# Performance work log

Hardware: AMD Instinct MI355X
Metric: run time of the kernel (lower is better)

## Reference

```python
import jax, jax.numpy as jnp
import numpy as np

D_MODEL = 1024
NUM_HEADS = 16
D_K = D_MODEL // NUM_HEADS


def setup_inputs() -> dict:
    key = jax.random.key(0)
    ks = jax.random.split(key, 9)
    B, S = 4, 2048
    scale = 1.0 / np.sqrt(D_MODEL)
    x = jax.random.normal(ks[0], (B, S, D_MODEL), dtype=jnp.float32)
    wq = jax.random.normal(ks[1], (D_MODEL, D_MODEL), dtype=jnp.float32) * scale
    wk = jax.random.normal(ks[2], (D_MODEL, D_MODEL), dtype=jnp.float32) * scale
    wv = jax.random.normal(ks[3], (D_MODEL, D_MODEL), dtype=jnp.float32) * scale
    wo = jax.random.normal(ks[4], (D_MODEL, D_MODEL), dtype=jnp.float32) * scale
    bq = jax.random.normal(ks[5], (D_MODEL,), dtype=jnp.float32) * 0.01
    bk = jax.random.normal(ks[6], (D_MODEL,), dtype=jnp.float32) * 0.01
    bv = jax.random.normal(ks[7], (D_MODEL,), dtype=jnp.float32) * 0.01
    bo = jax.random.normal(ks[8], (D_MODEL,), dtype=jnp.float32) * 0.01
    return {"x": x, "wq": wq, "bq": bq, "wk": wk, "bk": bk,
            "wv": wv, "bv": bv, "wo": wo, "bo": bo}


def reference(x, wq, bq, wk, bk, wv, bv, wo, bo):
    B, S, _ = x.shape
    # projections -> [B, H, S, d_k]
    def split_heads(t):
        return t.reshape(B, S, NUM_HEADS, D_K).transpose(0, 2, 1, 3)
    q = split_heads(x @ wq.T + bq)
    k = split_heads(x @ wk.T + bk)
    v = split_heads(x @ wv.T + bv)
    scores = jnp.einsum("bhqd,bhkd->bhqk", q, k) / np.sqrt(D_K).astype(np.float32)
    attn = jax.nn.softmax(scores, axis=-1)  # dropout is identity at eval
    out = jnp.einsum("bhqk,bhkd->bhqd", attn, v)
    out = out.transpose(0, 2, 1, 3).reshape(B, S, D_MODEL)
    return out @ wo.T + bo
```

## Files before the change

kernel.cpp:

```cpp
#include <hip/hip_runtime.h>

#define D_MODEL 1024
#define NHEADS  16
#define DK      64
#define BATCH   4
#define SEQ     2048
#define MROWS   (BATCH*SEQ)
#define BHCOUNT (BATCH*NHEADS)
#define KTILES  (SEQ/64)

typedef _Float16 half8 __attribute__((ext_vector_type(8)));
typedef _Float16 half4 __attribute__((ext_vector_type(4)));
typedef float    floatx4 __attribute__((ext_vector_type(4)));
typedef float    floatx16 __attribute__((ext_vector_type(16)));

__device__ __forceinline__ void load_lds16(const void* g, void* l) {
    __builtin_amdgcn_global_load_lds((const __attribute__((address_space(1))) void*)g,
                                     (__attribute__((address_space(3))) void*)l, 16, 0, 0);
}

__device__ __forceinline__ unsigned pkrtz_u32(float a, float b) {
    auto h = __builtin_amdgcn_cvt_pkrtz(a, b);
    union { decltype(h) v; unsigned u; } c; c.v = h; return c.u;
}

__device__ __forceinline__ int permrow(int r) {
    return (r & ~12) | ((r & 4) << 1) | ((r & 8) >> 1);
}

__global__ __launch_bounds__(256)
void cvt_f32_f16(const float* __restrict__ in, _Float16* __restrict__ out) {
    size_t i = ((size_t)blockIdx.x*256 + threadIdx.x)*4;
    float4 v = *(const float4*)(in + i);
    half4 h = {(_Float16)v.x, (_Float16)v.y, (_Float16)v.z, (_Float16)v.w};
    *(half4*)(out + i) = h;
}

__global__ __launch_bounds__(256)
void cvt4_f32_f16(const float* __restrict__ a, const float* __restrict__ b,
                  const float* __restrict__ c, const float* __restrict__ d,
                  _Float16* __restrict__ oa, _Float16* __restrict__ ob,
                  _Float16* __restrict__ oc, _Float16* __restrict__ od) {
    const float* src; _Float16* dst;
    switch (blockIdx.y) {
        case 0:  src=a; dst=oa; break;
        case 1:  src=b; dst=ob; break;
        case 2:  src=c; dst=oc; break;
        default: src=d; dst=od; break;
    }
    size_t i = ((size_t)blockIdx.x*256 + threadIdx.x)*4;
    float4 v = *(const float4*)(src + i);
    half4 h = {(_Float16)v.x, (_Float16)v.y, (_Float16)v.z, (_Float16)v.w};
    *(half4*)(dst + i) = h;
}

template<int MODE, int BK>
__global__ __launch_bounds__(256)
void gemm_nt_f16(const _Float16* __restrict__ A, const _Float16* __restrict__ W,
                 const float* __restrict__ b0, const float* __restrict__ b1,
                 const float* __restrict__ b2, void* __restrict__ Cout, float qscale)
{
    constexpr int GR  = BK/8;
    constexpr int NIT = BK/16;
    constexpr int NKT = 1024/BK;
    constexpr int KS  = BK/32;
    __shared__ _Float16 As[2][128*BK];
    __shared__ _Float16 Ws[2][128*BK];
    const int t = threadIdx.x;
    const int w = t >> 6, l = t & 63;
    const int wm = w >> 1, wn = w & 1;

    const int L   = blockIdx.x + (int)gridDim.x * blockIdx.y;
    const int nbx = gridDim.x;
    const int x   = L & 7;
    const int k   = L >> 3;
    const int cpc = (nbx + 7) >> 3;
    const int bn  = (x*cpc + (k % cpc)) * 128;
    const int bm  = (k / cpc) * 128;

    const int lrow = l & 15, lq4 = l >> 4;

    int srow[NIT], scol[NIT];
    #pragma unroll
    for (int it = 0; it < NIT; ++it) {
        int s = (it*4 + w)*64 + l;
        int r = s / GR, g = s % GR, gs;
        if constexpr (BK == 64) gs = g ^ (r & 7);
        else                    gs = g ^ ((r >> 1) & 3);
        srow[it] = r; scol[it] = gs*8;
    }

    floatx4 acc[4][4];
    #pragma unroll
    for (int i = 0; i < 4; ++i)
        #pragma unroll
        for (int j = 0; j < 4; ++j) acc[i][j] = (floatx4){0.f,0.f,0.f,0.f};

    #pragma unroll
    for (int it = 0; it < NIT; ++it) {
        load_lds16(A + (size_t)(bm + srow[it])*1024 + scol[it], &As[0][(it*4+w)*512]);
        load_lds16(W + (size_t)(bn + srow[it])*1024 + scol[it], &Ws[0][(it*4+w)*512]);
    }

    for (int kt = 0; kt < NKT; ++kt) {
        __syncthreads();
        const int cur = kt & 1;
        if (kt + 1 < NKT) {
            const int k1 = (kt + 1)*BK;
            #pragma unroll
            for (int it = 0; it < NIT; ++it) {
                load_lds16(A + (size_t)(bm + srow[it])*1024 + k1 + scol[it], &As[cur^1][(it*4+w)*512]);
                load_lds16(W + (size_t)(bn + srow[it])*1024 + k1 + scol[it], &Ws[cur^1][(it*4+w)*512]);
            }
        }
        #pragma unroll
        for (int ks = 0; ks < KS; ++ks) {
            int xg;
            if constexpr (BK == 64) xg = ((ks*4 + lq4) ^ (lrow & 7))*8;
            else                    xg = (lq4 ^ ((lrow >> 1) & 3))*8;
            half8 af[4], bf[4];
            #pragma unroll
            for (int i = 0; i < 4; ++i) af[i] = *(half8*)&As[cur][(wm*64 + i*16 + lrow)*BK + xg];
            #pragma unroll
            for (int j = 0; j < 4; ++j) bf[j] = *(half8*)&Ws[cur][(wn*64 + j*16 + lrow)*BK + xg];
            __builtin_amdgcn_s_setprio(1);
            #pragma unroll
            for (int i = 0; i < 4; ++i)
                #pragma unroll
                for (int j = 0; j < 4; ++j)
                    acc[i][j] = __builtin_amdgcn_mfma_f32_16x16x32_f16(af[i], bf[j], acc[i][j], 0, 0, 0);
            __builtin_amdgcn_s_setprio(0);
        }
    }

    constexpr size_t NXc = (size_t)MROWS * D_MODEL;
    const int which = bn >> 10;
    const float* bptr = (which == 0) ? b0 : (which == 1) ? b1 : b2;
    const float scale = (which == 0) ? qscale : 1.0f;
    #pragma unroll
    for (int j = 0; j < 4; ++j) {
        int gcol = bn + wn*64 + j*16 + lrow;
        float bv = bptr[gcol & 1023];
        #pragma unroll
        for (int i = 0; i < 4; ++i) {
            #pragma unroll
            for (int r = 0; r < 4; ++r) {
                int gm = bm + wm*64 + i*16 + lq4*4 + r;
                float val = (acc[i][j][r] + bv) * scale;
                if (MODE == 0) {
                    ((float*)Cout)[(size_t)gm*1024 + gcol] = val;
                } else {
                    int hc = gcol & 1023;
                    int b = gm >> 11, s = gm & 2047;
                    int h = hc >> 6, dk = hc & 63;
                    ((_Float16*)Cout)[which*NXc + (((size_t)(b*NHEADS + h))*SEQ + s)*DK + dk] = (_Float16)val;
                }
            }
        }
    }
}

__global__ __launch_bounds__(256)
void transpose_v(const _Float16* __restrict__ V, _Float16* __restrict__ Vt)
{
    __shared__ unsigned Lt[64][33];
    const int t = threadIdx.x;
    const int bh = blockIdx.y;
    const int s0 = blockIdx.x*64;
    const _Float16* Vb = V + ((size_t)bh*SEQ + s0)*DK;
    const int sp = t >> 3, dkc = (t & 7)*8;
    uint4 r0 = *(const uint4*)(Vb + (2*sp+0)*64 + dkc);
    uint4 r1 = *(const uint4*)(Vb + (2*sp+1)*64 + dkc);
    unsigned a0[4] = {r0.x, r0.y, r0.z, r0.w};
    unsigned a1[4] = {r1.x, r1.y, r1.z, r1.w};
    #pragma unroll
    for (int i = 0; i < 4; ++i) {
        Lt[dkc+2*i+0][sp] = (a0[i] & 0xFFFFu) | (a1[i] << 16);
        Lt[dkc+2*i+1][sp] = (a0[i] >> 16)     | (a1[i] & 0xFFFF0000u);
    }
    __syncthreads();
    const int dk = t >> 2, spc = (t & 3)*8;
    uint4 o0 = {Lt[dk][spc+0], Lt[dk][spc+1], Lt[dk][spc+2], Lt[dk][spc+3]};
    uint4 o1 = {Lt[dk][spc+4], Lt[dk][spc+5], Lt[dk][spc+6], Lt[dk][spc+7]};
    _Float16* dst = Vt + ((size_t)bh*DK + dk)*SEQ + s0 + spc*2;
    *(uint4*)(dst)     = o0;
    *(uint4*)(dst + 8) = o1;
}

__global__ __launch_bounds__(128)
void attn_mfma(const _Float16* __restrict__ Q, const _Float16* __restrict__ K,
               const _Float16* __restrict__ Vt, _Float16* __restrict__ AO)
{
    __shared__ _Float16 Ks[2][64*64];
    __shared__ _Float16 Vs[2][64*64];

    const int t = threadIdx.x;
    const int w = t >> 6, l = t & 63;
    const int l31 = l & 31, hi = l >> 5;

    const int L   = blockIdx.x + (int)gridDim.x * blockIdx.y;
    const int wid = (L & 7) * 128 + (L >> 3);
    const int bh  = wid >> 4;
    const int q0  = (wid & 15) * 128;

    const _Float16* Qb = Q  + ((size_t)bh*SEQ + q0)*DK;
    const _Float16* Kb = K  + (size_t)bh*SEQ*DK;
    const _Float16* Vb = Vt + (size_t)bh*DK*SEQ;

    int srow[4], scol[4], karow[4];
    #pragma unroll
    for (int it = 0; it < 4; ++it) {
        int s = (it*2 + w)*64 + l;
        int r = s >> 3;
        int lc = (s & 7) ^ (r & 7);
        srow[it] = r; scol[it] = lc*8;
        karow[it] = permrow(r);
    }

    half8 qf[2][4];
    #pragma unroll
    for (int qt = 0; qt < 2; ++qt)
        #pragma unroll
        for (int kk = 0; kk < 4; ++kk)
            qf[qt][kk] = *(const half8*)(Qb + (size_t)(w*64 + qt*32 + l31)*DK + kk*16 + hi*8);

    #pragma unroll
    for (int it = 0; it < 4; ++it) {
        load_lds16(Kb + (size_t)karow[it]*DK + scol[it], &Ks[0][(it*2+w)*512]);
        load_lds16(Vb + (size_t)srow[it]*SEQ + scol[it], &Vs[0][(it*2+w)*512]);
    }

    floatx16 Oacc[2][2];
    #pragma unroll
    for (int qt = 0; qt < 2; ++qt)
        #pragma unroll
        for (int i = 0; i < 16; ++i) { Oacc[qt][0][i] = 0.f; Oacc[qt][1][i] = 0.f; }
    float psum[2] = {0.f, 0.f};
    floatx16 z16;
    #pragma unroll
    for (int i = 0; i < 16; ++i) z16[i] = 0.f;

#define ATTN_PREFETCH(NBUF, KT1)                                                          \
    if ((KT1) < KTILES) {                                                                 \
        _Pragma("unroll")                                                                 \
        for (int it = 0; it < 4; ++it) {                                                  \
            load_lds16(Kb + ((size_t)((KT1)*64 + karow[it]))*DK + scol[it],               \
                       &Ks[NBUF][(it*2+w)*512]);                                          \
            load_lds16(Vb + (size_t)srow[it]*SEQ + (KT1)*64 + scol[it],                   \
                       &Vs[NBUF][(it*2+w)*512]);                                          \
        }                                                                                 \
    }

#define ATTN_STEP(CUR, KT)                                                                \
    {                                                                                     \
        __syncthreads();                                                                  \
        ATTN_PREFETCH((CUR)^1, (KT)+1)                                                    \
        _Pragma("unroll")                                                                 \
        for (int kb = 0; kb < 2; ++kb) {                                                  \
            const int row = kb*32 + l31;                                                  \
                                \
            floatx16 sTa, sTb;                                                            \
            {                                                                             \
                half8 kf = *(half8*)&Ks[CUR][row*64 + ((hi ^ (row & 7)))*8];              \
                sTa = __builtin_amdgcn_mfma_f32_32x32x16_f16(kf, qf[0][0], z16, 0, 0, 0); \
                sTb = __builtin_amdgcn_mfma_f32_32x32x16_f16(kf, qf[1][0], z16, 0, 0, 0); \
            }                                                                             \
            _Pragma("unroll")                                                             \
            for (int kk = 1; kk < 4; ++kk) {                                              \
                half8 kf = *(half8*)&Ks[CUR][row*64 + (((kk*2 + hi) ^ (row & 7)))*8];     \
                sTa = __builtin_amdgcn_mfma_f32_32x32x16_f16(kf, qf[0][kk], sTa, 0, 0, 0);\
                sTb = __builtin_amdgcn_mfma_f32_32x32x16_f16(kf, qf[1][kk], sTb, 0, 0, 0);\
            }                                                                             \
                     \
            unsigned Wda[8], Wdb[8];                                                      \
            _Pragma("unroll")                                                             \
            for (int p = 0; p < 8; ++p) {                                                 \
                float a0 = __builtin_amdgcn_exp2f(sTa[2*p]);                              \
                float a1 = __builtin_amdgcn_exp2f(sTa[2*p+1]);                            \
                psum[0] += a0 + a1;                                                       \
                Wda[p] = pkrtz_u32(a0, a1);                                               \
                float b0 = __builtin_amdgcn_exp2f(sTb[2*p]);                              \
                float b1 = __builtin_amdgcn_exp2f(sTb[2*p+1]);                            \
                psum[1] += b0 + b1;                                                       \
                Wdb[p] = pkrtz_u32(b0, b1);                                               \
            }                                                                             \
                                                   \
            _Pragma("unroll")                                                             \
            for (int kk2 = 0; kk2 < 2; ++kk2) {                                           \
                union { unsigned u[4]; half8 h; } pfa, pfb;                               \
                _Pragma("unroll")                                                         \
                for (int v = 0; v < 4; ++v) { pfa.u[v] = Wda[kk2*4 + v];                  \
                                              pfb.u[v] = Wdb[kk2*4 + v]; }                \
                const int vg = kb*4 + kk2*2 + hi;                                         \
                _Pragma("unroll")                                                         \
                for (int n = 0; n < 2; ++n) {                                             \
                    const int vrow = n*32 + l31;                                          \
                    half8 vf = *(half8*)&Vs[CUR][vrow*64 + ((vg ^ (vrow & 7)))*8];        \
                    Oacc[0][n] = __builtin_amdgcn_mfma_f32_32x32x16_f16(pfa.h, vf, Oacc[0][n], 0, 0, 0); \
                    Oacc[1][n] = __builtin_amdgcn_mfma_f32_32x32x16_f16(pfb.h, vf, Oacc[1][n], 0, 0, 0); \
                }                                                                         \
            }                                                                             \
        }                                                                                 \
    }

    for (int ktp = 0; ktp < KTILES; ktp += 2) {
        ATTN_STEP(0, ktp)
        ATTN_STEP(1, ktp+1)
    }
#undef ATTN_STEP
#undef ATTN_PREFETCH

    const int b = bh >> 4, h = bh & 15;
    #pragma unroll
    for (int qt = 0; qt < 2; ++qt) {
        float lsum = psum[qt] + __shfl_xor(psum[qt], 32, 64);
        float inv = 1.f / lsum;
        #pragma unroll
        for (int r = 0; r < 16; ++r) {
            int qrow = (r & 3) + 8*(r >> 2) + 4*hi;
            float invr = __shfl(inv, qrow, 64);
            int gq = q0 + w*64 + qt*32 + qrow;
            _Float16* dst = AO + ((size_t)(b*SEQ + gq))*D_MODEL + h*DK;
            dst[l31]      = (_Float16)(Oacc[qt][0][r] * invr);
            dst[32 + l31] = (_Float16)(Oacc[qt][1][r] * invr);
        }
    }
}

extern "C" void kernel_launch(void* const* d_in, const int* in_sizes, int n_in,
                              void* d_out, int out_size, void* d_ws, size_t ws_size,
                              hipStream_t stream)
{
    const float* x  = (const float*)d_in[0];
    const float* wq = (const float*)d_in[1];
    const float* bq = (const float*)d_in[2];
    const float* wk = (const float*)d_in[3];
    const float* bk = (const float*)d_in[4];
    const float* wv = (const float*)d_in[5];
    const float* bv = (const float*)d_in[6];
    const float* wo = (const float*)d_in[7];
    const float* bo = (const float*)d_in[8];

    const size_t NX = (size_t)MROWS * D_MODEL;
    const size_t NW = (size_t)D_MODEL * D_MODEL;
    _Float16* xh  = (_Float16*)d_ws;
    _Float16* wqh = xh  + NX;
    _Float16* wkh = wqh + NW;
    _Float16* wvh = wkh + NW;
    _Float16* woh = wvh + NW;
    _Float16* Qh  = woh + NW;
    _Float16* Kh  = Qh  + NX;
    _Float16* Vh  = Kh  + NX;
    _Float16* Vth = Vh  + NX;
    _Float16* AOh = Vth + NX;

    cvt_f32_f16<<<NX/1024, 256, 0, stream>>>(x, xh);
    cvt4_f32_f16<<<dim3(NW/1024, 4), 256, 0, stream>>>(wq, wk, wv, wo, wqh, wkh, wvh, woh);

    const float QSCALE = 0.125f * 1.44269504f;

    gemm_nt_f16<1,32><<<dim3(3*D_MODEL/128, MROWS/128), 256, 0, stream>>>(
        xh, wqh, bq, bk, bv, Qh, QSCALE);

    transpose_v<<<dim3(SEQ/64, BHCOUNT), 256, 0, stream>>>(Vh, Vth);
    attn_mfma<<<dim3(SEQ/128, BHCOUNT), 128, 0, stream>>>(Qh, Kh, Vth, AOh);

    gemm_nt_f16<0,64><<<dim3(D_MODEL/128, MROWS/128), 256, 0, stream>>>(
        AOh, woh, bo, bo, bo, d_out, 1.0f);
}
```

Baseline: 305.0 us.

## Add 256x256-tile 512-thread QKV projection GEMM kernel

Replaces the 128x128-tile QKV projection GEMM with a dedicated kernel using 256x256 tiles, 8 waves, BK=64 double buffering, and staged quarter-tile prefetches interleaved with MFMA sub-blocks. The larger tile raises arithmetic intensity and cuts global/L2 traffic per output, at the cost of 128KB LDS and high register pressure (128 accumulator floats per lane), which limits occupancy to one block per CU. The grid becomes 12x32 blocks with a remapped XCD-aware block ordering. The output GEMM is simplified to a plain fp32 bias epilogue.

```diff
diff --git a/kernel.cpp b/kernel.cpp
--- a/kernel.cpp
+++ b/kernel.cpp
@@ -54,11 +54,119 @@
     *(half4*)(dst + i) = h;
 }
 
-template<int MODE, int BK>
+__global__ __launch_bounds__(512)
+void gemm_qkv256(const _Float16* __restrict__ A, const _Float16* __restrict__ W,
+                 const float* __restrict__ b0, const float* __restrict__ b1,
+                 const float* __restrict__ b2, _Float16* __restrict__ Cout,
+                 float qscale)
+{
+    __shared__ _Float16 As[2][256*64];
+    __shared__ _Float16 Ws[2][256*64];
+    const int t = threadIdx.x;
+    const int w = t >> 6, l = t & 63;
+    const int wm = w >> 2, wn = w & 3;
+    const int lrow = l & 15, lq4 = l >> 4;
+
+    const int L   = blockIdx.x + (int)gridDim.x * blockIdx.y;
+    const int cpx = (int)(gridDim.x * gridDim.y) >> 3;
+    const int wid = (L & 7) * cpx + (L >> 3);
+    const int bn  = (wid % (int)gridDim.x) * 256;
+    const int bm  = (wid / (int)gridDim.x) * 256;
+
+    int srow[2], scol[2];
+    #pragma unroll
+    for (int it = 0; it < 2; ++it) {
+        int s = it*512 + t;
+        int r = s >> 3, g = s & 7;
+        srow[it] = r; scol[it] = (g ^ (r & 7))*8;
+    }
+
+    floatx4 acc[8][4];
+    #pragma unroll
+    for (int i = 0; i < 8; ++i)
+        #pragma unroll
+        for (int j = 0; j < 4; ++j) acc[i][j] = (floatx4){0.f,0.f,0.f,0.f};
+
+#define QKV_STAGE(P, KT1, NB)                                                          \
+    {                                                                                  \
+        const _Float16* sb = ((P) >> 1)                                                \
+            ? (W + (size_t)(bn + ((P)&1)*128)*1024)                                    \
+            : (A + (size_t)(bm + ((P)&1)*128)*1024);                                   \
+        _Float16* db = ((P) >> 1) ? &Ws[NB][0] : &As[NB][0];                           \
+        _Pragma("unroll")                                                              \
+        for (int it = 0; it < 2; ++it)                                                 \
+            load_lds16(sb + (size_t)srow[it]*1024 + (KT1)*64 + scol[it],               \
+                       db + ((P)&1)*8192 + (it*512 + w*64)*8);                         \
+    }
+
+    QKV_STAGE(0, 0, 0) QKV_STAGE(1, 0, 0) QKV_STAGE(2, 0, 0) QKV_STAGE(3, 0, 0)
+
+    for (int kt = 0; kt < 16; ++kt) {
+        const int cur = kt & 1;
+        __syncthreads();
+        #pragma unroll
+        for (int p = 0; p < 4; ++p) {
+            if (kt + 1 < 16) {
+                if      (p == 0) QKV_STAGE(0, kt+1, cur^1)
+                else if (p == 1) QKV_STAGE(1, kt+1, cur^1)
+                else if (p == 2) QKV_STAGE(2, kt+1, cur^1)
+                else             QKV_STAGE(3, kt+1, cur^1)
+            }
+            const int qm = p & 1, qn = p >> 1;
+            half8 af[4][2], bf[2][2];
+            #pragma unroll
+            for (int i = 0; i < 4; ++i)
+                #pragma unroll
+                for (int ks = 0; ks < 2; ++ks)
+                    af[i][ks] = *(half8*)&As[cur][(wm*128 + (qm*4+i)*16 + lrow)*64
+                                                  + (((ks*4 + lq4) ^ (lrow & 7)))*8];
+            #pragma unroll
+            for (int j = 0; j < 2; ++j)
+                #pragma unroll
+                for (int ks = 0; ks < 2; ++ks)
+                    bf[j][ks] = *(half8*)&Ws[cur][(wn*64 + (qn*2+j)*16 + lrow)*64
+                                                  + (((ks*4 + lq4) ^ (lrow & 7)))*8];
+            __builtin_amdgcn_s_setprio(1);
+            #pragma unroll
+            for (int i = 0; i < 4; ++i)
+                #pragma unroll
+                for (int j = 0; j < 2; ++j)
+                    #pragma unroll
+                    for (int ks = 0; ks < 2; ++ks)
+                        acc[qm*4+i][qn*2+j] = __builtin_amdgcn_mfma_f32_16x16x32_f16(
+                            af[i][ks], bf[j][ks], acc[qm*4+i][qn*2+j], 0, 0, 0);
+            __builtin_amdgcn_s_setprio(0);
+        }
+    }
+#undef QKV_STAGE
+
+    constexpr size_t NXc = (size_t)MROWS * D_MODEL;
+    const int which = bn >> 10;
+    const float* bptr = (which == 0) ? b0 : (which == 1) ? b1 : b2;
+    const float scale = (which == 0) ? qscale : 1.0f;
+    #pragma unroll
+    for (int nj = 0; nj < 4; ++nj) {
+        int gcol = bn + wn*64 + nj*16 + lrow;
+        float bv = bptr[gcol & 1023];
+        int hc = gcol & 1023;
+        int h = hc >> 6, dk = hc & 63;
+        #pragma unroll
+        for (int mi = 0; mi < 8; ++mi) {
+            #pragma unroll
+            for (int r = 0; r < 4; ++r) {
+                int gm = bm + wm*128 + mi*16 + lq4*4 + r;
+                int b = gm >> 11, s = gm & 2047;
+                Cout[which*NXc + (((size_t)(b*NHEADS + h))*SEQ + s)*DK + dk] =
+                    (_Float16)((acc[mi][nj][r] + bv) * scale);
+            }
+        }
+    }
+}
+
+template<int BK>
 __global__ __launch_bounds__(256)
 void gemm_nt_f16(const _Float16* __restrict__ A, const _Float16* __restrict__ W,
-                 const float* __restrict__ b0, const float* __restrict__ b1,
-                 const float* __restrict__ b2, void* __restrict__ Cout, float qscale)
+                 const float* __restrict__ bias, float* __restrict__ Cout)
 {
     constexpr int GR  = BK/8;
     constexpr int NIT = BK/16;
@@ -133,28 +241,16 @@
         }
     }
 
-    constexpr size_t NXc = (size_t)MROWS * D_MODEL;
-    const int which = bn >> 10;
-    const float* bptr = (which == 0) ? b0 : (which == 1) ? b1 : b2;
-    const float scale = (which == 0) ? qscale : 1.0f;
     #pragma unroll
     for (int j = 0; j < 4; ++j) {
         int gcol = bn + wn*64 + j*16 + lrow;
-        float bv = bptr[gcol & 1023];
+        float bv = bias[gcol];
         #pragma unroll
         for (int i = 0; i < 4; ++i) {
             #pragma unroll
             for (int r = 0; r < 4; ++r) {
                 int gm = bm + wm*64 + i*16 + lq4*4 + r;
-                float val = (acc[i][j][r] + bv) * scale;
-                if (MODE == 0) {
-                    ((float*)Cout)[(size_t)gm*1024 + gcol] = val;
-                } else {
-                    int hc = gcol & 1023;
-                    int b = gm >> 11, s = gm & 2047;
-                    int h = hc >> 6, dk = hc & 63;
-                    ((_Float16*)Cout)[which*NXc + (((size_t)(b*NHEADS + h))*SEQ + s)*DK + dk] = (_Float16)val;
-                }
+                Cout[(size_t)gm*1024 + gcol] = acc[i][j][r] + bv;
             }
         }
     }
@@ -258,7 +354,6 @@
         _Pragma("unroll")                                                                 \
         for (int kb = 0; kb < 2; ++kb) {                                                  \
             const int row = kb*32 + l31;                                                  \
-                                \
             floatx16 sTa, sTb;                                                            \
             {                                                                             \
                 half8 kf = *(half8*)&Ks[CUR][row*64 + ((hi ^ (row & 7)))*8];              \
@@ -271,7 +366,6 @@
                 sTa = __builtin_amdgcn_mfma_f32_32x32x16_f16(kf, qf[0][kk], sTa, 0, 0, 0);\
                 sTb = __builtin_amdgcn_mfma_f32_32x32x16_f16(kf, qf[1][kk], sTb, 0, 0, 0);\
             }                                                                             \
-                     \
             unsigned Wda[8], Wdb[8];                                                      \
             _Pragma("unroll")                                                             \
             for (int p = 0; p < 8; ++p) {                                                 \
@@ -284,7 +378,6 @@
                 psum[1] += b0 + b1;                                                       \
                 Wdb[p] = pkrtz_u32(b0, b1);                                               \
             }                                                                             \
-                                                   \
             _Pragma("unroll")                                                             \
             for (int kk2 = 0; kk2 < 2; ++kk2) {                                           \
                 union { unsigned u[4]; half8 h; } pfa, pfb;                               \
@@ -359,12 +452,12 @@
 
     const float QSCALE = 0.125f * 1.44269504f;
 
-    gemm_nt_f16<1,32><<<dim3(3*D_MODEL/128, MROWS/128), 256, 0, stream>>>(
+    gemm_qkv256<<<dim3(3*D_MODEL/256, MROWS/256), 512, 0, stream>>>(
         xh, wqh, bq, bk, bv, Qh, QSCALE);
 
     transpose_v<<<dim3(SEQ/64, BHCOUNT), 256, 0, stream>>>(Vh, Vth);
     attn_mfma<<<dim3(SEQ/128, BHCOUNT), 128, 0, stream>>>(Qh, Kh, Vth, AOh);
 
-    gemm_nt_f16<0,64><<<dim3(D_MODEL/128, MROWS/128), 256, 0, stream>>>(
-        AOh, woh, bo, bo, bo, d_out, 1.0f);
-}
+    gemm_nt_f16<64><<<dim3(D_MODEL/128, MROWS/128), 256, 0, stream>>>(
+        AOh, woh, bo, (float*)d_out);
+}
```

Result: slower. 320.7 us (+5.2%).

## Use triple-buffered LDS pipeline with explicit vmcnt waits in GEMM

Applied to the files above, without the earlier changes.

Replaces the double-buffered GEMM main loop with a three-stage LDS ring of BK=32 tiles. Each step waits on vmcnt, issues a raw s_barrier, and prefetches two tiles ahead, where the old loop synchronised fully every iteration. The output projection now also uses BK=32 instead of 64. The aim is deeper overlap of global loads with MFMA work and less barrier stall. The cost is more LDS per block, which may lower occupancy, and a hand-tuned vmcnt count that must match the number of issued loads exactly.

```diff
diff --git a/kernel.cpp b/kernel.cpp
--- a/kernel.cpp
+++ b/kernel.cpp
@@ -54,18 +54,14 @@
     *(half4*)(dst + i) = h;
 }
 
-template<int MODE, int BK>
+template<int MODE>
 __global__ __launch_bounds__(256)
 void gemm_nt_f16(const _Float16* __restrict__ A, const _Float16* __restrict__ W,
                  const float* __restrict__ b0, const float* __restrict__ b1,
                  const float* __restrict__ b2, void* __restrict__ Cout, float qscale)
 {
-    constexpr int GR  = BK/8;
-    constexpr int NIT = BK/16;
-    constexpr int NKT = 1024/BK;
-    constexpr int KS  = BK/32;
-    __shared__ _Float16 As[2][128*BK];
-    __shared__ _Float16 Ws[2][128*BK];
+    __shared__ _Float16 As[3][128*32];
+    __shared__ _Float16 Ws[3][128*32];
     const int t = threadIdx.x;
     const int w = t >> 6, l = t & 63;
     const int wm = w >> 1, wn = w & 1;
@@ -79,15 +75,14 @@
     const int bm  = (k / cpc) * 128;
 
     const int lrow = l & 15, lq4 = l >> 4;
-
-    int srow[NIT], scol[NIT];
-    #pragma unroll
-    for (int it = 0; it < NIT; ++it) {
+    const int xg = (lq4 ^ ((lrow >> 1) & 3))*8;
+
+    int srow[2], scol[2];
+    #pragma unroll
+    for (int it = 0; it < 2; ++it) {
         int s = (it*4 + w)*64 + l;
-        int r = s / GR, g = s % GR, gs;
-        if constexpr (BK == 64) gs = g ^ (r & 7);
-        else                    gs = g ^ ((r >> 1) & 3);
-        srow[it] = r; scol[it] = gs*8;
+        int r = s >> 2, g = s & 3;
+        srow[it] = r; scol[it] = (g ^ ((r >> 1) & 3))*8;
     }
 
     floatx4 acc[4][4];
@@ -96,42 +91,59 @@
         #pragma unroll
         for (int j = 0; j < 4; ++j) acc[i][j] = (floatx4){0.f,0.f,0.f,0.f};
 
-    #pragma unroll
-    for (int it = 0; it < NIT; ++it) {
-        load_lds16(A + (size_t)(bm + srow[it])*1024 + scol[it], &As[0][(it*4+w)*512]);
-        load_lds16(W + (size_t)(bn + srow[it])*1024 + scol[it], &Ws[0][(it*4+w)*512]);
-    }
-
-    for (int kt = 0; kt < NKT; ++kt) {
-        __syncthreads();
-        const int cur = kt & 1;
-        if (kt + 1 < NKT) {
-            const int k1 = (kt + 1)*BK;
-            #pragma unroll
-            for (int it = 0; it < NIT; ++it) {
-                load_lds16(A + (size_t)(bm + srow[it])*1024 + k1 + scol[it], &As[cur^1][(it*4+w)*512]);
-                load_lds16(W + (size_t)(bn + srow[it])*1024 + k1 + scol[it], &Ws[cur^1][(it*4+w)*512]);
-            }
-        }
-        #pragma unroll
-        for (int ks = 0; ks < KS; ++ks) {
-            int xg;
-            if constexpr (BK == 64) xg = ((ks*4 + lq4) ^ (lrow & 7))*8;
-            else                    xg = (lq4 ^ ((lrow >> 1) & 3))*8;
-            half8 af[4], bf[4];
-            #pragma unroll
-            for (int i = 0; i < 4; ++i) af[i] = *(half8*)&As[cur][(wm*64 + i*16 + lrow)*BK + xg];
-            #pragma unroll
-            for (int j = 0; j < 4; ++j) bf[j] = *(half8*)&Ws[cur][(wn*64 + j*16 + lrow)*BK + xg];
-            __builtin_amdgcn_s_setprio(1);
-            #pragma unroll
-            for (int i = 0; i < 4; ++i)
-                #pragma unroll
-                for (int j = 0; j < 4; ++j)
-                    acc[i][j] = __builtin_amdgcn_mfma_f32_16x16x32_f16(af[i], bf[j], acc[i][j], 0, 0, 0);
-            __builtin_amdgcn_s_setprio(0);
-        }
-    }
+#define GSTAGE(BUF, KT)                                                                \
+    {                                                                                  \
+        const int kc = (KT)*32;                                                        \
+        _Pragma("unroll")                                                              \
+        for (int it = 0; it < 2; ++it) {                                               \
+            load_lds16(A + (size_t)(bm + srow[it])*1024 + kc + scol[it],               \
+                       &As[BUF][(it*4+w)*512]);                                        \
+            load_lds16(W + (size_t)(bn + srow[it])*1024 + kc + scol[it],               \
+                       &Ws[BUF][(it*4+w)*512]);                                        \
+        }                                                                              \
+    }
+
+#define GCOMPUTE(CUR)                                                                  \
+    {                                                                                  \
+        half8 af[4], bf[4];                                                            \
+        _Pragma("unroll")                                                              \
+        for (int i = 0; i < 4; ++i)                                                    \
+            af[i] = *(half8*)&As[CUR][(wm*64 + i*16 + lrow)*32 + xg];                  \
+        _Pragma("unroll")                                                              \
+        for (int j = 0; j < 4; ++j)                                                    \
+            bf[j] = *(half8*)&Ws[CUR][(wn*64 + j*16 + lrow)*32 + xg];                  \
+        __builtin_amdgcn_s_setprio(1);                                                 \
+        _Pragma("unroll")                                                              \
+        for (int i = 0; i < 4; ++i)                                                    \
+            _Pragma("unroll")                                                          \
+            for (int j = 0; j < 4; ++j)                                                \
+                acc[i][j] = __builtin_amdgcn_mfma_f32_16x16x32_f16(af[i], bf[j],       \
+                                                                   acc[i][j], 0, 0, 0);\
+        __builtin_amdgcn_s_setprio(0);                                                 \
+    }
+
+#define GSTEP(CUR, SBUF, KT, VMSTR)                                                    \
+    {                                                                                  \
+        asm volatile("s_waitcnt vmcnt(" VMSTR ")" ::: "memory");                       \
+        __builtin_amdgcn_s_barrier();                                                  \
+        __builtin_amdgcn_sched_barrier(0);                                             \
+        if ((KT) + 2 < 32) GSTAGE(SBUF, (KT)+2)                                        \
+        GCOMPUTE(CUR)                                                                  \
+    }
+
+    GSTAGE(0, 0)
+    GSTAGE(1, 1)
+
+    for (int kt0 = 0; kt0 < 30; kt0 += 3) {
+        GSTEP(0, 2, kt0,   "4")
+        GSTEP(1, 0, kt0+1, "4")
+        GSTEP(2, 1, kt0+2, "4")
+    }
+    GSTEP(0, 2, 30, "4")
+    GSTEP(1, 2, 31, "0")
+#undef GSTEP
+#undef GCOMPUTE
+#undef GSTAGE
 
     constexpr size_t NXc = (size_t)MROWS * D_MODEL;
     const int which = bn >> 10;
@@ -258,7 +270,6 @@
         _Pragma("unroll")                                                                 \
         for (int kb = 0; kb < 2; ++kb) {                                                  \
             const int row = kb*32 + l31;                                                  \
-                                \
             floatx16 sTa, sTb;                                                            \
             {                                                                             \
                 half8 kf = *(half8*)&Ks[CUR][row*64 + ((hi ^ (row & 7)))*8];              \
@@ -271,7 +282,6 @@
                 sTa = __builtin_amdgcn_mfma_f32_32x32x16_f16(kf, qf[0][kk], sTa, 0, 0, 0);\
                 sTb = __builtin_amdgcn_mfma_f32_32x32x16_f16(kf, qf[1][kk], sTb, 0, 0, 0);\
             }                                                                             \
-                     \
             unsigned Wda[8], Wdb[8];                                                      \
             _Pragma("unroll")                                                             \
             for (int p = 0; p < 8; ++p) {                                                 \
@@ -284,7 +294,6 @@
                 psum[1] += b0 + b1;                                                       \
                 Wdb[p] = pkrtz_u32(b0, b1);                                               \
             }                                                                             \
-                                                   \
             _Pragma("unroll")                                                             \
             for (int kk2 = 0; kk2 < 2; ++kk2) {                                           \
                 union { unsigned u[4]; half8 h; } pfa, pfb;                               \
@@ -359,12 +368,12 @@
 
     const float QSCALE = 0.125f * 1.44269504f;
 
-    gemm_nt_f16<1,32><<<dim3(3*D_MODEL/128, MROWS/128), 256, 0, stream>>>(
+    gemm_nt_f16<1><<<dim3(3*D_MODEL/128, MROWS/128), 256, 0, stream>>>(
         xh, wqh, bq, bk, bv, Qh, QSCALE);
 
     transpose_v<<<dim3(SEQ/64, BHCOUNT), 256, 0, stream>>>(Vh, Vth);
     attn_mfma<<<dim3(SEQ/128, BHCOUNT), 128, 0, stream>>>(Qh, Kh, Vth, AOh);
 
-    gemm_nt_f16<0,64><<<dim3(D_MODEL/128, MROWS/128), 256, 0, stream>>>(
+    gemm_nt_f16<0><<<dim3(D_MODEL/128, MROWS/128), 256, 0, stream>>>(
         AOh, woh, bo, bo, bo, d_out, 1.0f);
 }
```

Measured after the change: 309.9 us. About the same (+1.6%).
